# Kernel tuning notes

Measured on AMD Instinct MI355X. Metric: run time of the kernel, lower is better.

## Reference

```python
import jax, jax.numpy as jnp
import numpy as np

EMBED_DIM = 32
DELTA_V = 0.5
DELTA_D = 3.0
NUM_LABELS = 20  # instance labels are 1..NUM_LABELS; 0 is background


def _safe_sqrt(x):
    # sqrt with zero-safe gradient (matches norm of identical points -> 0)
    s = jnp.where(x > 0, x, 1.0)
    return jnp.where(x > 0, jnp.sqrt(s), 0.0)


def _per_batch(emb, seg):
    # emb: [D, N], seg: [N] int labels in 0..L (0 = background)
    D, N = emb.shape
    L = NUM_LABELS
    dt = emb.dtype
    ones = jnp.ones((N,), dt)
    counts = jax.ops.segment_sum(ones, seg, num_segments=L + 1)          # [L+1]
    sums = jax.ops.segment_sum(emb.T, seg, num_segments=L + 1)          # [L+1, D]
    means = sums / jnp.maximum(counts, 1.0)[:, None]                     # [L+1, D]
    present = (counts > 0).at[0].set(False)                              # [L+1]
    num_lanes = jnp.sum(present.astype(dt))

    # --- variance (pull) loss: each pixel vs its own instance centroid ---
    mpix = means[seg]                                                    # [N, D] gather
    sq = jnp.sum((emb.T - mpix) ** 2, axis=1)                            # [N]
    d = _safe_sqrt(sq)
    v = jnp.maximum(d - DELTA_V, 0.0) ** 2 * (seg > 0).astype(dt)        # background excluded
    vsum = jax.ops.segment_sum(v, seg, num_segments=L + 1)               # [L+1]
    vmean = vsum / jnp.maximum(counts, 1.0)
    var_loss = jnp.sum(vmean * present.astype(dt)) / jnp.maximum(num_lanes, 1.0)
    var_loss = jnp.where(num_lanes > 0, var_loss, jnp.zeros((), dt))

    # --- distance (push) loss between present centroids ---
    m = means[1:]                                                        # [L, D]
    p = present[1:]                                                      # [L]
    sqd = jnp.sum((m[:, None, :] - m[None, :, :]) ** 2, axis=-1)         # [L, L]
    dist = _safe_sqrt(sqd)
    pair = (p[:, None] & p[None, :]) & ~jnp.eye(L, dtype=bool)
    dl = jnp.sum(jnp.maximum(DELTA_D - dist, 0.0) ** 2 * pair.astype(dt))
    denom = jnp.maximum(num_lanes * (num_lanes - 1.0), 1.0)
    dist_loss = jnp.where(num_lanes > 1, dl / denom / 2.0, jnp.zeros((), dt))
    return var_loss, dist_loss


def setup_inputs() -> dict:
    key = jax.random.key(0)
    k1, k2 = jax.random.split(key)
    B, D, N = 8, EMBED_DIM, 65536  # 256x256 BEV raster flattened
    embedding = jax.random.normal(k1, (B, D, N), dtype=jnp.float32)
    seg_gt = jax.random.randint(k2, (B, N), 0, NUM_LABELS + 1, dtype=jnp.int32)
    return {"embedding": embedding, "seg_gt": seg_gt}


def reference(embedding, seg_gt):
    var_b, dist_b = jax.vmap(_per_batch)(embedding, seg_gt)  # [B], [B]
    var_loss = jnp.mean(var_b)
    dist_loss = jnp.mean(dist_b)
    reg_loss = jnp.zeros((), embedding.dtype)
    return (var_loss, dist_loss, reg_loss)
```

## Files before the change

kernel.cpp:

```cpp
#include <hip/hip_runtime.h>
#include <hip/hip_cooperative_groups.h>
namespace cg = cooperative_groups;

#define NSEG 21
#define NLBL 20
#define DIM  32
#define NS   128
#define NREP 16
#define DV   0.5f
#define DD   3.0f
#define BATCH 8
#define N_PIX 65536

using short8 = __attribute__((ext_vector_type(8))) short;
using f32x4  = __attribute__((ext_vector_type(4))) float;

#define P_OFF  0
#define C2_OFF 655360
#define M_OFF  675840
#define CN_OFF 680960
#define V_OFF  681120
#define PB_OFF 701600

__device__ __forceinline__ short bf16rne(float f) {
  const unsigned u = __builtin_bit_cast(unsigned, f);
  return (short)((u + 0x7FFFu + ((u >> 16) & 1u)) >> 16);
}

__device__ __forceinline__ void momentsBody(const float* __restrict__ emb,
                                            const int* __restrict__ seg,
                                            float* __restrict__ ws,
                                            float* lred, int bx, int b, int tid) {
  const int wv = tid >> 6, lane = tid & 63;
  const int lr = lane & 15, lg = lane >> 4;
  const float* rowA0 = emb + ((size_t)b * DIM + lr) * N_PIX;
  const float* rowA1 = rowA0 + (size_t)16 * N_PIX;
  const int*   segb  = seg + (size_t)b * N_PIX;

  f32x4 s00 = {0,0,0,0}, s01 = {0,0,0,0}, s10 = {0,0,0,0}, s11 = {0,0,0,0};
  f32x4 c0  = {0,0,0,0}, c1  = {0,0,0,0};
  short8 ones;
  #pragma unroll
  for (int j = 0; j < 8; ++j) ones[j] = (short)0x3F80;

  const int nbase = bx * 512 + wv * 32;
  #pragma unroll 2
  for (int t = 0; t < 4; ++t) {
    const int koff = nbase + t * 128 + lg * 8;
    const float4 a00 = *(const float4*)(rowA0 + koff);
    const float4 a01 = *(const float4*)(rowA0 + koff + 4);
    const float4 a10 = *(const float4*)(rowA1 + koff);
    const float4 a11 = *(const float4*)(rowA1 + koff + 4);
    const int4   g0  = *(const int4*)(segb + koff);
    const int4   g1  = *(const int4*)(segb + koff + 4);

    short8 fa0, fa1, fb0, fb1;
    fa0[0] = bf16rne(a00.x); fa0[1] = bf16rne(a00.y);
    fa0[2] = bf16rne(a00.z); fa0[3] = bf16rne(a00.w);
    fa0[4] = bf16rne(a01.x); fa0[5] = bf16rne(a01.y);
    fa0[6] = bf16rne(a01.z); fa0[7] = bf16rne(a01.w);
    fa1[0] = bf16rne(a10.x); fa1[1] = bf16rne(a10.y);
    fa1[2] = bf16rne(a10.z); fa1[3] = bf16rne(a10.w);
    fa1[4] = bf16rne(a11.x); fa1[5] = bf16rne(a11.y);
    fa1[6] = bf16rne(a11.z); fa1[7] = bf16rne(a11.w);
    const int lab0 = lr + 1, lab1 = lr + 17;
    fb0[0] = (g0.x == lab0) ? (short)0x3F80 : (short)0;
    fb0[1] = (g0.y == lab0) ? (short)0x3F80 : (short)0;
    fb0[2] = (g0.z == lab0) ? (short)0x3F80 : (short)0;
    fb0[3] = (g0.w == lab0) ? (short)0x3F80 : (short)0;
    fb0[4] = (g1.x == lab0) ? (short)0x3F80 : (short)0;
    fb0[5] = (g1.y == lab0) ? (short)0x3F80 : (short)0;
    fb0[6] = (g1.z == lab0) ? (short)0x3F80 : (short)0;
    fb0[7] = (g1.w == lab0) ? (short)0x3F80 : (short)0;
    fb1[0] = (g0.x == lab1) ? (short)0x3F80 : (short)0;
    fb1[1] = (g0.y == lab1) ? (short)0x3F80 : (short)0;
    fb1[2] = (g0.z == lab1) ? (short)0x3F80 : (short)0;
    fb1[3] = (g0.w == lab1) ? (short)0x3F80 : (short)0;
    fb1[4] = (g1.x == lab1) ? (short)0x3F80 : (short)0;
    fb1[5] = (g1.y == lab1) ? (short)0x3F80 : (short)0;
    fb1[6] = (g1.z == lab1) ? (short)0x3F80 : (short)0;
    fb1[7] = (g1.w == lab1) ? (short)0x3F80 : (short)0;

    s00 = __builtin_amdgcn_mfma_f32_16x16x32_bf16(fa0, fb0, s00, 0, 0, 0);
    s01 = __builtin_amdgcn_mfma_f32_16x16x32_bf16(fa0, fb1, s01, 0, 0, 0);
    s10 = __builtin_amdgcn_mfma_f32_16x16x32_bf16(fa1, fb0, s10, 0, 0, 0);
    s11 = __builtin_amdgcn_mfma_f32_16x16x32_bf16(fa1, fb1, s11, 0, 0, 0);
    c0  = __builtin_amdgcn_mfma_f32_16x16x32_bf16(ones, fb0, c0, 0, 0, 0);
    c1  = __builtin_amdgcn_mfma_f32_16x16x32_bf16(ones, fb1, c1, 0, 0, 0);
  }

  float vals[24];
  #pragma unroll
  for (int r = 0; r < 4; ++r) {
    vals[0 * 4 + r] = s00[r]; vals[1 * 4 + r] = s01[r];
    vals[2 * 4 + r] = s10[r]; vals[3 * 4 + r] = s11[r];
    vals[4 * 4 + r] = c0[r];  vals[5 * 4 + r] = c1[r];
  }
  #pragma unroll
  for (int w = 0; w < 4; ++w) {
    if (wv == w) {
      float* base = lred + lane * 4;
      if (w == 0) {
        #pragma unroll
        for (int f = 0; f < 6; ++f) {
          #pragma unroll
          for (int r = 0; r < 4; ++r) base[f * 256 + r] = vals[f * 4 + r];
        }
      } else {
        #pragma unroll
        for (int f = 0; f < 6; ++f) {
          #pragma unroll
          for (int r = 0; r < 4; ++r) base[f * 256 + r] += vals[f * 4 + r];
        }
      }
    }
    __syncthreads();
  }
  for (int i = tid; i < 1536; i += 256) {
    const float v = lred[i];
    const int f = i >> 8, ln = (i >> 2) & 63, r = i & 3;
    const int col = ln & 15, row = ((ln >> 4) << 2) | r;
    if (f < 4) {
      const int d = (f >> 1) * 16 + row;
      const int lcol = (f & 1) * 16 + col;
      if (lcol < NLBL)
        ws[P_OFF + (((size_t)(b * DIM + d) * NLBL) + lcol) * NS + bx] = v;
    } else {
      const int lcol = (f & 1) * 16 + col;
      if (row == 0 && lcol < NLBL)
        ws[C2_OFF + ((size_t)b * NLBL + lcol) * NS + bx] = v;
    }
  }
}

__device__ __forceinline__ void meansBody(float* __restrict__ ws, float* s_c,
                                          int bx8, int b, int tid) {
  if (tid < NLBL) {
    const float4* cp = (const float4*)(ws + C2_OFF + ((size_t)b * NLBL + tid) * NS);
    float q0 = 0.f, q1 = 0.f, q2 = 0.f, q3 = 0.f;
    #pragma unroll
    for (int k = 0; k < NS / 4; k += 4) {
      const float4 v0 = cp[k], v1 = cp[k + 1], v2 = cp[k + 2], v3 = cp[k + 3];
      q0 += v0.x + v0.y + v0.z + v0.w;
      q1 += v1.x + v1.y + v1.z + v1.w;
      q2 += v2.x + v2.y + v2.z + v2.w;
      q3 += v3.x + v3.y + v3.z + v3.w;
    }
    const float c = q0 + q1 + q2 + q3;
    if (bx8 == 0) ws[CN_OFF + b * NLBL + tid] = c;
    s_c[tid] = fmaxf(c, 1.f);
  }
  __syncthreads();
  if (tid < 80) {
    const int m = bx8 * 80 + tid;
    const int l = m >> 5;
    const int d = m & 31;
    const float4* pp = (const float4*)(ws + P_OFF + (((size_t)(b * DIM + d) * NLBL) + l) * NS);
    float q0 = 0.f, q1 = 0.f, q2 = 0.f, q3 = 0.f;
    #pragma unroll
    for (int k = 0; k < NS / 4; k += 4) {
      const float4 v0 = pp[k], v1 = pp[k + 1], v2 = pp[k + 2], v3 = pp[k + 3];
      q0 += v0.x + v0.y + v0.z + v0.w;
      q1 += v1.x + v1.y + v1.z + v1.w;
      q2 += v2.x + v2.y + v2.z + v2.w;
      q3 += v3.x + v3.y + v3.z + v3.w;
    }
    ws[M_OFF + (size_t)b * NLBL * DIM + m] = (q0 + q1 + q2 + q3) / s_c[l];
  }
}

__device__ __forceinline__ void varBody(const float* __restrict__ emb,
                                        const int* __restrict__ seg,
                                        float* __restrict__ ws,
                                        float* s_m, float* s_v,
                                        int bx, int b, int tid) {
  for (int i = tid; i < NSEG * 33; i += 256) s_m[i] = 0.f;
  for (int i = tid; i < NREP * NSEG; i += 256) s_v[i] = 0.f;
  __syncthreads();
  if (tid < 160) {
    const float4 v = ((const float4*)(ws + M_OFF + (size_t)b * NLBL * DIM))[tid];
    const int flat = tid * 4, l = flat >> 5, d = flat & 31;
    float* dst = &s_m[(l + 1) * 33 + d];
    dst[0] = v.x; dst[1] = v.y; dst[2] = v.z; dst[3] = v.w;
  }
  __syncthreads();

  const int n0 = bx * 512;
  const int2 sl = ((const int2*)(seg + (size_t)b * N_PIX + n0))[tid];
  const float2* e2 = (const float2*)(emb + (size_t)b * DIM * N_PIX + n0) + tid;
  const int mx = sl.x * 33, my = sl.y * 33;
  float q0 = 0.f, q1 = 0.f;
  #pragma unroll 8
  for (int d = 0; d < DIM; ++d) {
    const float2 e = e2[d * (N_PIX / 2)];
    float t;
    t = e.x - s_m[mx + d]; q0 += t * t;
    t = e.y - s_m[my + d]; q1 += t * t;
  }
  const int rb = (tid & (NREP - 1)) * NSEG;
  if (sl.x > 0) { const float r = sqrtf(q0) - DV; if (r > 0.f) atomicAdd(&s_v[rb + sl.x], r * r); }
  if (sl.y > 0) { const float r = sqrtf(q1) - DV; if (r > 0.f) atomicAdd(&s_v[rb + sl.y], r * r); }
  __syncthreads();
  if (tid < NLBL) {
    float v = 0.f;
    #pragma unroll
    for (int r = 0; r < NREP; ++r) v += s_v[r * NSEG + (tid + 1)];
    ws[V_OFF + ((size_t)b * NLBL + tid) * NS + bx] = v;
  }
}

__device__ __forceinline__ void finalBody(float* __restrict__ ws,
                                          float* s_m, float* s_c, float* s_vs,
                                          int* s_p, float* s_red, int b, int tid) {
  const int wv = tid >> 6, lane = tid & 63;
  if (tid < 160) {
    const int g = tid >> 3, j = tid & 7;
    const float4* v4 = (const float4*)(ws + V_OFF + ((size_t)b * NLBL + g) * NS + j * 16);
    float s = 0.f;
    #pragma unroll
    for (int k = 0; k < 4; ++k) { const float4 v = v4[k]; s += v.x + v.y + v.z + v.w; }
    s += __shfl_xor(s, 1, 64); s += __shfl_xor(s, 2, 64); s += __shfl_xor(s, 4, 64);
    if (j == 0) s_vs[g] = s;
  }
  if (tid < NLBL) {
    const float c = ws[CN_OFF + b * NLBL + tid];
    s_c[tid] = c;
    s_p[tid] = (c > 0.f) ? 1 : 0;
  }
  if (tid < 160) {
    const float4 v = ((const float4*)(ws + M_OFF + (size_t)b * NLBL * DIM))[tid];
    const int flat = tid * 4, l = flat >> 5, d = flat & 31;
    float* dst = &s_m[l * 33 + d];
    dst[0] = v.x; dst[1] = v.y; dst[2] = v.z; dst[3] = v.w;
  }
  __syncthreads();

  float dl = 0.f;
  for (int p = tid; p < NLBL * NLBL; p += 256) {
    const int i = p / NLBL, j = p - (p / NLBL) * NLBL;
    if (i != j && s_p[i] && s_p[j]) {
      float sq = 0.f;
      #pragma unroll
      for (int d = 0; d < DIM; ++d) {
        const float t = s_m[i * 33 + d] - s_m[j * 33 + d];
        sq += t * t;
      }
      const float r = DD - sqrtf(sq);
      if (r > 0.f) dl += r * r;
    }
  }
  #pragma unroll
  for (int off = 32; off; off >>= 1) dl += __shfl_xor(dl, off, 64);
  if (lane == 0) s_red[wv] = dl;
  __syncthreads();
  if (tid == 0) {
    const float dsum = s_red[0] + s_red[1] + s_red[2] + s_red[3];
    float nl = 0.f, var = 0.f;
    for (int l = 0; l < NLBL; ++l)
      if (s_p[l]) { nl += 1.f; var += s_vs[l] / s_c[l]; }
    ws[PB_OFF + b * 2]     = (nl > 0.f) ? var / nl : 0.f;
    ws[PB_OFF + b * 2 + 1] = (nl > 1.f) ? dsum / fmaxf(nl * (nl - 1.f), 1.f) * 0.5f : 0.f;
  }
}

__device__ __forceinline__ void outBody(const float* __restrict__ ws,
                                        float* __restrict__ out, int tid) {
  if (tid < 64) {
    float v = 0.f, d = 0.f;
    if (tid < BATCH) {
      v = ws[PB_OFF + tid * 2];
      d = ws[PB_OFF + tid * 2 + 1];
    }
    #pragma unroll
    for (int off = 4; off; off >>= 1) { v += __shfl_xor(v, off, 64); d += __shfl_xor(d, off, 64); }
    if (tid == 0) {
      out[0] = v / (float)BATCH;
      out[1] = d / (float)BATCH;
      out[2] = 0.f;
    }
  }
}

__global__ __launch_bounds__(256, 4)
void k_fused(const float* __restrict__ emb, const int* __restrict__ seg,
             float* __restrict__ ws, float* __restrict__ out) {
  __shared__ float lred[1536];
  __shared__ float s_m[NSEG * 33];
  __shared__ float s_v[NREP * NSEG];
  __shared__ float s_c[NLBL];
  __shared__ float s_vs[NLBL];
  __shared__ int   s_p[NLBL];
  __shared__ float s_red[4];
  cg::grid_group gg = cg::this_grid();
  const int tid = threadIdx.x, bx = blockIdx.x, b = blockIdx.y;

  momentsBody(emb, seg, ws, lred, bx, b, tid);
  gg.sync();
  if (bx < 8) meansBody(ws, s_c, bx, b, tid);
  gg.sync();
  varBody(emb, seg, ws, s_m, s_v, bx, b, tid);
  gg.sync();
  if (bx == 0) finalBody(ws, s_m, s_c, s_vs, s_p, s_red, b, tid);
  gg.sync();
  if (bx == 0 && b == 0) outBody(ws, out, tid);
}

__global__ __launch_bounds__(256)
void k_moments(const float* __restrict__ emb, const int* __restrict__ seg,
               float* __restrict__ ws) {
  __shared__ float lred[1536];
  momentsBody(emb, seg, ws, lred, blockIdx.x, blockIdx.y, threadIdx.x);
}
__global__ __launch_bounds__(256)
void k_means(float* __restrict__ ws) {
  __shared__ float s_c[NLBL];
  meansBody(ws, s_c, blockIdx.x, blockIdx.y, threadIdx.x);
}
__global__ __launch_bounds__(256)
void k_var(const float* __restrict__ emb, const int* __restrict__ seg,
           float* __restrict__ ws) {
  __shared__ float s_m[NSEG * 33];
  __shared__ float s_v[NREP * NSEG];
  varBody(emb, seg, ws, s_m, s_v, blockIdx.x, blockIdx.y, threadIdx.x);
}
__global__ __launch_bounds__(256)
void k_final(float* __restrict__ ws) {
  __shared__ float s_m[NLBL * 33];
  __shared__ float s_c[NLBL];
  __shared__ float s_vs[NLBL];
  __shared__ int   s_p[NLBL];
  __shared__ float s_red[4];
  finalBody(ws, s_m, s_c, s_vs, s_p, s_red, blockIdx.x, threadIdx.x);
}
__global__ __launch_bounds__(64)
void k_out(const float* __restrict__ ws, float* __restrict__ out) {
  outBody(ws, out, threadIdx.x);
}

extern "C" void kernel_launch(void* const* d_in, const int* in_sizes, int n_in,
                              void* d_out, int out_size, void* d_ws, size_t ws_size,
                              hipStream_t stream) {
  const float* emb = (const float*)d_in[0];
  const int*   seg = (const int*)d_in[1];
  float* out = (float*)d_out;
  float* ws  = (float*)d_ws;

  int maxB = 0;
  bool coop = false;
  if (hipOccupancyMaxActiveBlocksPerMultiprocessor(&maxB, (const void*)k_fused, 256, 0)
        == hipSuccess)
    coop = ((long)maxB * 256 >= (long)NS * BATCH);
  if (coop) {
    void* args[] = {(void*)&emb, (void*)&seg, (void*)&ws, (void*)&out};
    if (hipLaunchCooperativeKernel((const void*)k_fused, dim3(NS, BATCH), dim3(256),
                                   args, 0, stream) == hipSuccess)
      return;
  }
  k_moments<<<dim3(NS, BATCH), 256, 0, stream>>>(emb, seg, ws);
  k_means  <<<dim3(8, BATCH), 256, 0, stream>>>(ws);
  k_var    <<<dim3(NS, BATCH), 256, 0, stream>>>(emb, seg, ws);
  k_final  <<<dim3(BATCH), 256, 0, stream>>>(ws);
  k_out    <<<1, 64, 0, stream>>>(ws, out);
}
```

Baseline: 48.04 us.

## Cache bf16 embedding tile in LDS to reuse in variance pass

During the moments pass each block now stores its bf16-converted embedding slice (XOR-swizzled) and packed byte labels in dynamic LDS. The fused kernel's variance stage reads from that LDS tile instead of reading the fp32 embedding from global memory a second time. Blocks per batch are halved so each block covers 1024 pixels, with launch bounds lowered to 2 blocks/CU to fit about 66 KB of dynamic LDS. The aim is to remove the second full HBM pass over the embedding. The cost is lower occupancy, and the variance distances are now computed from bf16-rounded embeddings rather than fp32 values.

```diff
diff --git a/kernel.cpp b/kernel.cpp
--- a/kernel.cpp
+++ b/kernel.cpp
@@ -5,22 +5,24 @@
 #define NSEG 21
 #define NLBL 20
 #define DIM  32
-#define NS   128
+#define NS   64
 #define NREP 16
 #define DV   0.5f
 #define DD   3.0f
 #define BATCH 8
 #define N_PIX 65536
+#define SMS  36
+#define DYNB (128*512 + 1024)
 
 using short8 = __attribute__((ext_vector_type(8))) short;
 using f32x4  = __attribute__((ext_vector_type(4))) float;
 
 #define P_OFF  0
-#define C2_OFF 655360
-#define M_OFF  675840
-#define CN_OFF 680960
-#define V_OFF  681120
-#define PB_OFF 701600
+#define C2_OFF (BATCH*DIM*NLBL*NS)
+#define M_OFF  (C2_OFF + BATCH*NLBL*NS)
+#define CN_OFF (M_OFF + BATCH*NLBL*DIM)
+#define V_OFF  (CN_OFF + BATCH*NLBL)
+#define PB_OFF (V_OFF + BATCH*NLBL*NS)
 
 __device__ __forceinline__ short bf16rne(float f) {
   const unsigned u = __builtin_bit_cast(unsigned, f);
@@ -30,7 +32,9 @@
 __device__ __forceinline__ void momentsBody(const float* __restrict__ emb,
                                             const int* __restrict__ seg,
                                             float* __restrict__ ws,
-                                            float* lred, int bx, int b, int tid) {
+                                            float* lred, ushort* tile,
+                                            unsigned char* segt,
+                                            int bx, int b, int tid) {
   const int wv = tid >> 6, lane = tid & 63;
   const int lr = lane & 15, lg = lane >> 4;
   const float* rowA0 = emb + ((size_t)b * DIM + lr) * N_PIX;
@@ -43,10 +47,10 @@
   #pragma unroll
   for (int j = 0; j < 8; ++j) ones[j] = (short)0x3F80;
 
-  const int nbase = bx * 512 + wv * 32;
   #pragma unroll 2
-  for (int t = 0; t < 4; ++t) {
-    const int koff = nbase + t * 128 + lg * 8;
+  for (int t = 0; t < 8; ++t) {
+    const int kl = wv * 256 + t * 32 + lg * 8;
+    const int koff = bx * 1024 + kl;
     const float4 a00 = *(const float4*)(rowA0 + koff);
     const float4 a01 = *(const float4*)(rowA0 + koff + 4);
     const float4 a10 = *(const float4*)(rowA1 + koff);
@@ -81,6 +85,18 @@
     fb1[6] = (g1.z == lab1) ? (short)0x3F80 : (short)0;
     fb1[7] = (g1.w == lab1) ? (short)0x3F80 : (short)0;
 
+    const int o = kl >> 3, om = o & 7;
+    *(short8*)&tile[o * 256 + ((lr ^ om) << 3)] = fa0;
+    *(short8*)&tile[o * 256 + (((lr ^ om) + 16) << 3)] = fa1;
+    if (lr == 0) {
+      unsigned long long pk =
+          (unsigned long long)(g0.x & 255)        | ((unsigned long long)(g0.y & 255) << 8) |
+          ((unsigned long long)(g0.z & 255) << 16) | ((unsigned long long)(g0.w & 255) << 24) |
+          ((unsigned long long)(g1.x & 255) << 32) | ((unsigned long long)(g1.y & 255) << 40) |
+          ((unsigned long long)(g1.z & 255) << 48) | ((unsigned long long)(g1.w & 255) << 56);
+      *(unsigned long long*)&segt[o * 8] = pk;
+    }
+
     s00 = __builtin_amdgcn_mfma_f32_16x16x32_bf16(fa0, fb0, s00, 0, 0, 0);
     s01 = __builtin_amdgcn_mfma_f32_16x16x32_bf16(fa0, fb1, s01, 0, 0, 0);
     s10 = __builtin_amdgcn_mfma_f32_16x16x32_bf16(fa1, fb0, s10, 0, 0, 0);
@@ -102,16 +118,14 @@
       float* base = lred + lane * 4;
       if (w == 0) {
         #pragma unroll
-        for (int f = 0; f < 6; ++f) {
+        for (int f = 0; f < 6; ++f)
           #pragma unroll
           for (int r = 0; r < 4; ++r) base[f * 256 + r] = vals[f * 4 + r];
-        }
       } else {
         #pragma unroll
-        for (int f = 0; f < 6; ++f) {
+        for (int f = 0; f < 6; ++f)
           #pragma unroll
           for (int r = 0; r < 4; ++r) base[f * 256 + r] += vals[f * 4 + r];
-        }
       }
     }
     __syncthreads();
@@ -153,8 +167,7 @@
   __syncthreads();
   if (tid < 80) {
     const int m = bx8 * 80 + tid;
-    const int l = m >> 5;
-    const int d = m & 31;
+    const int l = m >> 5, d = m & 31;
     const float4* pp = (const float4*)(ws + P_OFF + (((size_t)(b * DIM + d) * NLBL) + l) * NS);
     float q0 = 0.f, q1 = 0.f, q2 = 0.f, q3 = 0.f;
     #pragma unroll
@@ -169,43 +182,15 @@
   }
 }
 
-__device__ __forceinline__ void varBody(const float* __restrict__ emb,
-                                        const int* __restrict__ seg,
-                                        float* __restrict__ ws,
-                                        float* s_m, float* s_v,
-                                        int bx, int b, int tid) {
-  for (int i = tid; i < NSEG * 33; i += 256) s_m[i] = 0.f;
-  for (int i = tid; i < NREP * NSEG; i += 256) s_v[i] = 0.f;
+__device__ __forceinline__ void loadMeans(const float* __restrict__ ws,
+                                          float* s_m, int b, int tid) {
+  for (int i = tid; i < NSEG * SMS; i += 256) s_m[i] = 0.f;
   __syncthreads();
   if (tid < 160) {
     const float4 v = ((const float4*)(ws + M_OFF + (size_t)b * NLBL * DIM))[tid];
     const int flat = tid * 4, l = flat >> 5, d = flat & 31;
-    float* dst = &s_m[(l + 1) * 33 + d];
+    float* dst = &s_m[(l + 1) * SMS + d];
     dst[0] = v.x; dst[1] = v.y; dst[2] = v.z; dst[3] = v.w;
-  }
-  __syncthreads();
-
-  const int n0 = bx * 512;
-  const int2 sl = ((const int2*)(seg + (size_t)b * N_PIX + n0))[tid];
-  const float2* e2 = (const float2*)(emb + (size_t)b * DIM * N_PIX + n0) + tid;
-  const int mx = sl.x * 33, my = sl.y * 33;
-  float q0 = 0.f, q1 = 0.f;
-  #pragma unroll 8
-  for (int d = 0; d < DIM; ++d) {
-    const float2 e = e2[d * (N_PIX / 2)];
-    float t;
-    t = e.x - s_m[mx + d]; q0 += t * t;
-    t = e.y - s_m[my + d]; q1 += t * t;
-  }
-  const int rb = (tid & (NREP - 1)) * NSEG;
-  if (sl.x > 0) { const float r = sqrtf(q0) - DV; if (r > 0.f) atomicAdd(&s_v[rb + sl.x], r * r); }
-  if (sl.y > 0) { const float r = sqrtf(q1) - DV; if (r > 0.f) atomicAdd(&s_v[rb + sl.y], r * r); }
-  __syncthreads();
-  if (tid < NLBL) {
-    float v = 0.f;
-    #pragma unroll
-    for (int r = 0; r < NREP; ++r) v += s_v[r * NSEG + (tid + 1)];
-    ws[V_OFF + ((size_t)b * NLBL + tid) * NS + bx] = v;
   }
 }
 
@@ -215,10 +200,9 @@
   const int wv = tid >> 6, lane = tid & 63;
   if (tid < 160) {
     const int g = tid >> 3, j = tid & 7;
-    const float4* v4 = (const float4*)(ws + V_OFF + ((size_t)b * NLBL + g) * NS + j * 16);
-    float s = 0.f;
-    #pragma unroll
-    for (int k = 0; k < 4; ++k) { const float4 v = v4[k]; s += v.x + v.y + v.z + v.w; }
+    const float4* v4 = (const float4*)(ws + V_OFF + ((size_t)b * NLBL + g) * NS + j * 8);
+    const float4 a = v4[0], c = v4[1];
+    float s = a.x + a.y + a.z + a.w + c.x + c.y + c.z + c.w;
     s += __shfl_xor(s, 1, 64); s += __shfl_xor(s, 2, 64); s += __shfl_xor(s, 4, 64);
     if (j == 0) s_vs[g] = s;
   }
@@ -227,12 +211,8 @@
     s_c[tid] = c;
     s_p[tid] = (c > 0.f) ? 1 : 0;
   }
-  if (tid < 160) {
-    const float4 v = ((const float4*)(ws + M_OFF + (size_t)b * NLBL * DIM))[tid];
-    const int flat = tid * 4, l = flat >> 5, d = flat & 31;
-    float* dst = &s_m[l * 33 + d];
-    dst[0] = v.x; dst[1] = v.y; dst[2] = v.z; dst[3] = v.w;
-  }
+  __syncthreads();
+  loadMeans(ws, s_m, b, tid);
   __syncthreads();
 
   float dl = 0.f;
@@ -242,7 +222,7 @@
       float sq = 0.f;
       #pragma unroll
       for (int d = 0; d < DIM; ++d) {
-        const float t = s_m[i * 33 + d] - s_m[j * 33 + d];
+        const float t = s_m[(i + 1) * SMS + d] - s_m[(j + 1) * SMS + d];
         sq += t * t;
       }
       const float r = DD - sqrtf(sq);
@@ -281,11 +261,14 @@
   }
 }
 
-__global__ __launch_bounds__(256, 4)
+__global__ __launch_bounds__(256, 2)
 void k_fused(const float* __restrict__ emb, const int* __restrict__ seg,
              float* __restrict__ ws, float* __restrict__ out) {
-  __shared__ float lred[1536];
-  __shared__ float s_m[NSEG * 33];
+  extern __shared__ __align__(16) char dynls[];
+  ushort* tile = (ushort*)dynls;
+  unsigned char* segt = (unsigned char*)(dynls + 65536);
+  __shared__ __align__(16) float lred[1536];
+  __shared__ __align__(16) float s_m[NSEG * SMS];
   __shared__ float s_v[NREP * NSEG];
   __shared__ float s_c[NLBL];
   __shared__ float s_vs[NLBL];
@@ -294,11 +277,49 @@
   cg::grid_group gg = cg::this_grid();
   const int tid = threadIdx.x, bx = blockIdx.x, b = blockIdx.y;
 
-  momentsBody(emb, seg, ws, lred, bx, b, tid);
+  momentsBody(emb, seg, ws, lred, tile, segt, bx, b, tid);
   gg.sync();
   if (bx < 8) meansBody(ws, s_c, bx, b, tid);
   gg.sync();
-  varBody(emb, seg, ws, s_m, s_v, bx, b, tid);
+
+  for (int i = tid; i < NREP * NSEG; i += 256) s_v[i] = 0.f;
+  loadMeans(ws, s_m, b, tid);
+  __syncthreads();
+  {
+    const int px0 = tid * 4;
+    const int o = px0 >> 3, om = o & 7, p8 = px0 & 7;
+    const int la0 = segt[px0], la1 = segt[px0 + 1], la2 = segt[px0 + 2], la3 = segt[px0 + 3];
+    float q0 = 0.f, q1 = 0.f, q2 = 0.f, q3 = 0.f;
+    #pragma unroll
+    for (int db = 0; db < 8; ++db) {
+      const f32x4 m0 = *(const f32x4*)&s_m[la0 * SMS + db * 4];
+      const f32x4 m1 = *(const f32x4*)&s_m[la1 * SMS + db * 4];
+      const f32x4 m2 = *(const f32x4*)&s_m[la2 * SMS + db * 4];
+      const f32x4 m3 = *(const f32x4*)&s_m[la3 * SMS + db * 4];
+      #pragma unroll
+      for (int dd = 0; dd < 4; ++dd) {
+        const int d = db * 4 + dd;
+        const ushort4 ev = *(const ushort4*)&tile[o * 256 + ((d ^ om) << 3) + p8];
+        float t;
+        t = __builtin_bit_cast(float, (unsigned)ev.x << 16) - m0[dd]; q0 += t * t;
+        t = __builtin_bit_cast(float, (unsigned)ev.y << 16) - m1[dd]; q1 += t * t;
+        t = __builtin_bit_cast(float, (unsigned)ev.z << 16) - m2[dd]; q2 += t * t;
+        t = __builtin_bit_cast(float, (unsigned)ev.w << 16) - m3[dd]; q3 += t * t;
+      }
+    }
+    const int rb = (tid & (NREP - 1)) * NSEG;
+    if (la0 > 0) { const float r = sqrtf(q0) - DV; if (r > 0.f) atomicAdd(&s_v[rb + la0], r * r); }
+    if (la1 > 0) { const float r = sqrtf(q1) - DV; if (r > 0.f) atomicAdd(&s_v[rb + la1], r * r); }
+    if (la2 > 0) { const float r = sqrtf(q2) - DV; if (r > 0.f) atomicAdd(&s_v[rb + la2], r * r); }
+    if (la3 > 0) { const float r = sqrtf(q3) - DV; if (r > 0.f) atomicAdd(&s_v[rb + la3], r * r); }
+  }
+  __syncthreads();
+  if (tid < NLBL) {
+    float v = 0.f;
+    #pragma unroll
+    for (int r = 0; r < NREP; ++r) v += s_v[r * NSEG + (tid + 1)];
+    ws[V_OFF + ((size_t)b * NLBL + tid) * NS + bx] = v;
+  }
   gg.sync();
   if (bx == 0) finalBody(ws, s_m, s_c, s_vs, s_p, s_red, b, tid);
   gg.sync();
@@ -308,8 +329,11 @@
 __global__ __launch_bounds__(256)
 void k_moments(const float* __restrict__ emb, const int* __restrict__ seg,
                float* __restrict__ ws) {
-  __shared__ float lred[1536];
-  momentsBody(emb, seg, ws, lred, blockIdx.x, blockIdx.y, threadIdx.x);
+  extern __shared__ __align__(16) char dynls[];
+  ushort* tile = (ushort*)dynls;
+  unsigned char* segt = (unsigned char*)(dynls + 65536);
+  __shared__ __align__(16) float lred[1536];
+  momentsBody(emb, seg, ws, lred, tile, segt, blockIdx.x, blockIdx.y, threadIdx.x);
 }
 __global__ __launch_bounds__(256)
 void k_means(float* __restrict__ ws) {
@@ -317,15 +341,43 @@
   meansBody(ws, s_c, blockIdx.x, blockIdx.y, threadIdx.x);
 }
 __global__ __launch_bounds__(256)
-void k_var(const float* __restrict__ emb, const int* __restrict__ seg,
-           float* __restrict__ ws) {
-  __shared__ float s_m[NSEG * 33];
+void k_varG(const float* __restrict__ emb, const int* __restrict__ seg,
+            float* __restrict__ ws) {
+  __shared__ __align__(16) float s_m[NSEG * SMS];
   __shared__ float s_v[NREP * NSEG];
-  varBody(emb, seg, ws, s_m, s_v, blockIdx.x, blockIdx.y, threadIdx.x);
+  const int tid = threadIdx.x, bx = blockIdx.x, b = blockIdx.y;
+  for (int i = tid; i < NREP * NSEG; i += 256) s_v[i] = 0.f;
+  loadMeans(ws, s_m, b, tid);
+  __syncthreads();
+  const int n0 = bx * 1024 + tid * 4;
+  const int4 sl = *(const int4*)(seg + (size_t)b * N_PIX + n0);
+  const float4* e4 = (const float4*)(emb + (size_t)b * DIM * N_PIX + n0);
+  float q0 = 0.f, q1 = 0.f, q2 = 0.f, q3 = 0.f;
+  #pragma unroll 8
+  for (int d = 0; d < DIM; ++d) {
+    const float4 e = e4[d * (N_PIX / 4)];
+    float t;
+    t = e.x - s_m[sl.x * SMS + d]; q0 += t * t;
+    t = e.y - s_m[sl.y * SMS + d]; q1 += t * t;
+    t = e.z - s_m[sl.z * SMS + d]; q2 += t * t;
+    t = e.w - s_m[sl.w * SMS + d]; q3 += t * t;
+  }
+  const int rb = (tid & (NREP - 1)) * NSEG;
+  if (sl.x > 0) { const float r = sqrtf(q0) - DV; if (r > 0.f) atomicAdd(&s_v[rb + sl.x], r * r); }
+  if (sl.y > 0) { const float r = sqrtf(q1) - DV; if (r > 0.f) atomicAdd(&s_v[rb + sl.y], r * r); }
+  if (sl.z > 0) { const float r = sqrtf(q2) - DV; if (r > 0.f) atomicAdd(&s_v[rb + sl.z], r * r); }
+  if (sl.w > 0) { const float r = sqrtf(q3) - DV; if (r > 0.f) atomicAdd(&s_v[rb + sl.w], r * r); }
+  __syncthreads();
+  if (tid < NLBL) {
+    float v = 0.f;
+    #pragma unroll
+    for (int r = 0; r < NREP; ++r) v += s_v[r * NSEG + (tid + 1)];
+    ws[V_OFF + ((size_t)b * NLBL + tid) * NS + bx] = v;
+  }
 }
 __global__ __launch_bounds__(256)
 void k_final(float* __restrict__ ws) {
-  __shared__ float s_m[NLBL * 33];
+  __shared__ __align__(16) float s_m[NSEG * SMS];
   __shared__ float s_c[NLBL];
   __shared__ float s_vs[NLBL];
   __shared__ int   s_p[NLBL];
@@ -347,18 +399,18 @@
 
   int maxB = 0;
   bool coop = false;
-  if (hipOccupancyMaxActiveBlocksPerMultiprocessor(&maxB, (const void*)k_fused, 256, 0)
+  if (hipOccupancyMaxActiveBlocksPerMultiprocessor(&maxB, (const void*)k_fused, 256, DYNB)
         == hipSuccess)
     coop = ((long)maxB * 256 >= (long)NS * BATCH);
   if (coop) {
     void* args[] = {(void*)&emb, (void*)&seg, (void*)&ws, (void*)&out};
     if (hipLaunchCooperativeKernel((const void*)k_fused, dim3(NS, BATCH), dim3(256),
-                                   args, 0, stream) == hipSuccess)
+                                   args, DYNB, stream) == hipSuccess)
       return;
   }
-  k_moments<<<dim3(NS, BATCH), 256, 0, stream>>>(emb, seg, ws);
+  k_moments<<<dim3(NS, BATCH), 256, DYNB, stream>>>(emb, seg, ws);
   k_means  <<<dim3(8, BATCH), 256, 0, stream>>>(ws);
-  k_var    <<<dim3(NS, BATCH), 256, 0, stream>>>(emb, seg, ws);
+  k_varG   <<<dim3(NS, BATCH), 256, 0, stream>>>(emb, seg, ws);
   k_final  <<<dim3(BATCH), 256, 0, stream>>>(ws);
   k_out    <<<1, 64, 0, stream>>>(ws, out);
 }
```

After: 43.19 us. -10.1%, faster.
